# Optimization experiments

Measured on AMD Instinct MI355X. Metric: run time of the kernel, lower is better.

## Reference

```python
import jax, jax.numpy as jnp
import numpy as np

N_NODES = 50000
N_EDGES = 800000
HIDDEN = 128
IN_DIM = 128
OUT_DIM = 1
N_LAYERS = 4
N_GRAPHS = 32
LN_EPS = 1e-5


def setup_inputs() -> dict:
    key = jax.random.key(0)
    ks = jax.random.split(key, 12)
    s = 1.0 / np.sqrt(HIDDEN)
    inp = {
        "x": jax.random.normal(ks[0], (N_NODES, IN_DIM), dtype=jnp.float32),
        "edge_index": jax.random.randint(ks[1], (2, N_EDGES), 0, N_NODES, dtype=jnp.int64),
        "batch": jnp.sort(jax.random.randint(ks[2], (N_NODES,), 0, N_GRAPHS, dtype=jnp.int64)),
        "W_emb": jax.random.normal(ks[3], (HIDDEN, IN_DIM), dtype=jnp.float32) * s,
        "b_emb": jax.random.normal(ks[4], (HIDDEN,), dtype=jnp.float32) * s,
        "W_layers": jax.random.normal(ks[5], (N_LAYERS, HIDDEN, HIDDEN), dtype=jnp.float32) * s,
        "b_layers": jax.random.normal(ks[6], (N_LAYERS, HIDDEN), dtype=jnp.float32) * s,
        "ln_gamma": 1.0 + 0.02 * jax.random.normal(ks[7], (N_LAYERS, HIDDEN), dtype=jnp.float32),
        "ln_beta": 0.02 * jax.random.normal(ks[8], (N_LAYERS, HIDDEN), dtype=jnp.float32),
        "W_out": jax.random.normal(ks[9], (OUT_DIM, HIDDEN), dtype=jnp.float32) * s,
    }
    return inp


def _layer_norm(x, gamma, beta):
    mu = jnp.mean(x, axis=-1, keepdims=True)
    var = jnp.mean(jnp.square(x - mu), axis=-1, keepdims=True)
    return (x - mu) * jax.lax.rsqrt(var + LN_EPS) * gamma + beta


def reference(x, edge_index, batch, W_emb, b_emb, W_layers, b_layers, ln_gamma, ln_beta, W_out):
    n = x.shape[0]
    # add self-loops (PyG GCNConv default)
    loop = jnp.arange(n, dtype=edge_index.dtype)
    row = jnp.concatenate([edge_index[0], loop])  # source nodes
    col = jnp.concatenate([edge_index[1], loop])  # target nodes
    # symmetric normalization: deg over targets
    deg = jax.ops.segment_sum(jnp.ones_like(col, dtype=x.dtype), col, num_segments=n)
    dis = jnp.where(deg > 0, jax.lax.rsqrt(jnp.maximum(deg, 1.0)), 0.0)
    norm = dis[row] * dis[col]  # [E+N]

    h = x @ W_emb.T + b_emb  # embedding layer
    for i in range(N_LAYERS):
        t = h @ W_layers[i].T                      # [N, H] linear first
        msg = t[row] * norm[:, None]               # gather + scale  [E+N, H]
        agg = jax.ops.segment_sum(msg, col, num_segments=n) + b_layers[i]
        h = _layer_norm(h + jax.nn.relu(agg), ln_gamma[i], ln_beta[i])

    out = h @ W_out.T                              # [N, OUT_DIM]
    sums = jax.ops.segment_sum(out, batch, num_segments=N_GRAPHS)
    cnts = jax.ops.segment_sum(jnp.ones((n,), out.dtype), batch, num_segments=N_GRAPHS)
    return sums / jnp.maximum(cnts, 1.0)[:, None]  # [N_GRAPHS, OUT_DIM]
```

## Files before the change

kernel.cpp:

```cpp
#include <hip/hip_runtime.h>
#include <hip/hip_fp16.h>

#define NN 50000
#define NE 800000
#define NH 128
#define NG 32
#define NL 4
#define NB 196
#define WSLOT (NH * NH)

typedef __attribute__((ext_vector_type(8))) short bf16x8;
typedef __attribute__((ext_vector_type(4))) float f32x4;
typedef __attribute__((ext_vector_type(2))) float f32x2;

__device__ inline short f2bf(float x) {
  union { float f; unsigned u; } v;
  v.f = x;
  unsigned r = v.u + 0x7FFF + ((v.u >> 16) & 1);
  return (short)(r >> 16);
}
__device__ inline float bf2f(short s) {
  union { unsigned u; float f; } v;
  v.u = ((unsigned)(unsigned short)s) << 16;
  return v.f;
}

__device__ inline int block_exscan(int v) {
  __shared__ int wsum[4];
  int tid = threadIdx.x, wave = tid >> 6, lane = tid & 63;
  int x = v;
#pragma unroll
  for (int off = 1; off < 64; off <<= 1) {
    int y = __shfl_up(x, off, 64);
    if (lane >= off) x += y;
  }
  if (lane == 63) wsum[wave] = x;
  __syncthreads();
  int wp = 0;
  if (wave > 0) wp += wsum[0];
  if (wave > 1) wp += wsum[1];
  if (wave > 2) wp += wsum[2];
  return wp + x - v;
}

__global__ __launch_bounds__(256) void prep_swizzle(const float* __restrict__ W_emb,
                                                    const float* __restrict__ W_layers,
                                                    short* __restrict__ hi,
                                                    short* __restrict__ lo) {
  int i = blockIdx.x * 256 + threadIdx.x;
  if (i >= 5 * WSLOT) return;
  int slot = i >> 14, f = i & (WSLOT - 1);
  int j = f & 7, lane = (f >> 3) & 63, tt = (f >> 9) & 7, ks = f >> 12;
  int n = tt * 16 + (lane & 15);
  int k = ks * 32 + ((lane >> 4) & 3) * 8 + j;
  const float* W = slot ? (W_layers + (size_t)(slot - 1) * WSLOT) : W_emb;
  float x = W[n * NH + k];
  short hh = f2bf(x);
  hi[i] = hh;
  lo[i] = f2bf(x - bf2f(hh));
}

__global__ __launch_bounds__(256) void hist_kernel(const int* __restrict__ col,
                                                   int* __restrict__ cnt,
                                                   int* __restrict__ rank) {
  int e = blockIdx.x * 256 + threadIdx.x;
  if (e < NE) rank[e] = atomicAdd(&cnt[col[e]], 1);
}

__global__ __launch_bounds__(256) void scan1_kernel(const int* __restrict__ cnt,
                                                    int* __restrict__ bsum,
                                                    float* __restrict__ dis) {
  int i = blockIdx.x * 256 + threadIdx.x;
  int v = (i < NN) ? cnt[i] : 0;
  if (i < NN) dis[i] = rsqrtf((float)(v + 1));
  int lane = threadIdx.x & 63;
  int s = v;
#pragma unroll
  for (int off = 32; off; off >>= 1) s += __shfl_down(s, off, 64);
  __shared__ int ws[4];
  if (lane == 0) ws[threadIdx.x >> 6] = s;
  __syncthreads();
  if (threadIdx.x == 0) bsum[blockIdx.x] = ws[0] + ws[1] + ws[2] + ws[3];
}

__global__ __launch_bounds__(256) void scan2_kernel(const int* __restrict__ bsum,
                                                    int* __restrict__ ebsum) {
  int tid = threadIdx.x;
  int v = (tid < NB) ? bsum[tid] : 0;
  int ex = block_exscan(v);
  if (tid < NB) ebsum[tid] = ex;
}

__global__ __launch_bounds__(256) void scan3_kernel(const int* __restrict__ cnt,
                                                    const int* __restrict__ ebsum,
                                                    int* __restrict__ offs) {
  int i = blockIdx.x * 256 + threadIdx.x;
  int v = (i < NN) ? cnt[i] : 0;
  int ex = block_exscan(v);
  if (i < NN) offs[i] = ebsum[blockIdx.x] + ex;
}

__global__ __launch_bounds__(256) void fill_kernel(const int* __restrict__ row,
                                                   const int* __restrict__ col,
                                                   const int* __restrict__ rank,
                                                   const float* __restrict__ dis,
                                                   const int* __restrict__ offs,
                                                   int2* __restrict__ csr) {
  int e = blockIdx.x * 256 + threadIdx.x;
  if (e < NE) {
    int d = col[e];
    int s = row[e];
    int pos = offs[d] + rank[e];
    csr[pos] = make_int2(s, __float_as_int(dis[s] * dis[d]));
  }
}

template <bool EMB, bool LAST>
__global__ __launch_bounds__(512) void gemm_mfma(const float* __restrict__ Xf,
                                                 const __half* __restrict__ Xh,
                                                 const short* __restrict__ Whi,
                                                 const short* __restrict__ Wlo,
                                                 const float* __restrict__ bias,
                                                 const __half* __restrict__ hprev,
                                                 const float* __restrict__ gamma,
                                                 const float* __restrict__ beta,
                                                 const float* __restrict__ Wout,
                                                 __half* __restrict__ hnew,
                                                 unsigned char* __restrict__ h8,
                                                 float* __restrict__ nodeval) {
  __shared__ short Wh[WSLOT];
  __shared__ short Wl[WSLOT];
  int tid = threadIdx.x;
#pragma unroll
  for (int i = tid * 8; i < WSLOT; i += 512 * 8) {
    *(bf16x8*)&Wh[i] = *(const bf16x8*)(Whi + i);
    *(bf16x8*)&Wl[i] = *(const bf16x8*)(Wlo + i);
  }
  __syncthreads();

  int wave = tid >> 6, lane = tid & 63;
  int quad = lane >> 4, r16 = lane & 15;
  int m0 = blockIdx.x * 128 + wave * 16;
  if (m0 >= NN) return;
  int mA = m0 + r16;

  f32x4 acc[8];
#pragma unroll
  for (int t = 0; t < 8; ++t) acc[t] = (f32x4){0.f, 0.f, 0.f, 0.f};

#pragma unroll
  for (int ks = 0; ks < 4; ++ks) {
    int klane = ks * 32 + quad * 8;
    float af[8];
    if (EMB) {
      const float* xr = Xf + (size_t)mA * NH + klane;
      float4 a0 = *(const float4*)xr;
      float4 a1 = *(const float4*)(xr + 4);
      af[0] = a0.x; af[1] = a0.y; af[2] = a0.z; af[3] = a0.w;
      af[4] = a1.x; af[5] = a1.y; af[6] = a1.z; af[7] = a1.w;
    } else {
      const __half2* xr = (const __half2*)(Xh + (size_t)mA * NH + klane);
#pragma unroll
      for (int q = 0; q < 4; ++q) {
        float2 f = __half22float2(xr[q]);
        af[2 * q] = f.x;
        af[2 * q + 1] = f.y;
      }
    }
    bf16x8 xhi, xlo;
#pragma unroll
    for (int j = 0; j < 8; ++j) {
      short h = f2bf(af[j]);
      xhi[j] = h;
      xlo[j] = f2bf(af[j] - bf2f(h));
    }
#pragma unroll
    for (int t = 0; t < 8; ++t) {
      int fidx = ((ks * 8 + t) * 64 + lane) << 3;
      bf16x8 whi = *(const bf16x8*)&Wh[fidx];
      bf16x8 wlo = *(const bf16x8*)&Wl[fidx];
      acc[t] = __builtin_amdgcn_mfma_f32_16x16x32_bf16(whi, xhi, acc[t], 0, 0, 0);
      acc[t] = __builtin_amdgcn_mfma_f32_16x16x32_bf16(whi, xlo, acc[t], 0, 0, 0);
      acc[t] = __builtin_amdgcn_mfma_f32_16x16x32_bf16(wlo, xhi, acc[t], 0, 0, 0);
    }
  }

  int m = m0 + r16;
  int cb = quad * 4;
  if (EMB) {
#pragma unroll
    for (int t = 0; t < 8; ++t) {
      int ch = t * 16 + cb;
      float4 bb = *(const float4*)(bias + ch);
      float o0 = acc[t][0] + bb.x, o1 = acc[t][1] + bb.y;
      float o2 = acc[t][2] + bb.z, o3 = acc[t][3] + bb.w;
      __half2 p01 = __float22half2_rn(make_float2(o0, o1));
      __half2 p23 = __float22half2_rn(make_float2(o2, o3));
      *(uint2*)(hnew + (size_t)m * NH + ch) =
          make_uint2(*(unsigned*)&p01, *(unsigned*)&p23);
      int v = 0;
      v = __builtin_amdgcn_cvt_pk_fp8_f32(o0, o1, v, 0);
      v = __builtin_amdgcn_cvt_pk_fp8_f32(o2, o3, v, 1);
      ((unsigned*)(h8 + (size_t)m * NH))[t * 4 + quad] = (unsigned)v;
    }
  } else {
    float v[8][4];
    float s = 0.f, s2 = 0.f;
#pragma unroll
    for (int t = 0; t < 8; ++t) {
      int ch = t * 16 + cb;
      float4 bb = *(const float4*)(bias + ch);
      uint2 hp = *(const uint2*)(hprev + (size_t)m * NH + ch);
      float2 h01 = __half22float2(*(__half2*)&hp.x);
      float2 h23 = __half22float2(*(__half2*)&hp.y);
      float hv[4] = {h01.x, h01.y, h23.x, h23.y};
      float bb4[4] = {bb.x, bb.y, bb.z, bb.w};
#pragma unroll
      for (int r = 0; r < 4; ++r) {
        float z = fmaxf(acc[t][r] + bb4[r], 0.f);
        float val = hv[r] + z;
        v[t][r] = val;
        s += val;
        s2 += val * val;
      }
    }
    s += __shfl_xor(s, 16, 64);
    s += __shfl_xor(s, 32, 64);
    s2 += __shfl_xor(s2, 16, 64);
    s2 += __shfl_xor(s2, 32, 64);
    float mean = s * (1.f / 128.f);
    float var = fmaxf(s2 * (1.f / 128.f) - mean * mean, 0.f);
    float inv = rsqrtf(var + 1e-5f);
    float d = 0.f;
#pragma unroll
    for (int t = 0; t < 8; ++t) {
      int ch = t * 16 + cb;
      float4 gv = *(const float4*)(gamma + ch);
      float4 bt = *(const float4*)(beta + ch);
      float o0 = (v[t][0] - mean) * inv * gv.x + bt.x;
      float o1 = (v[t][1] - mean) * inv * gv.y + bt.y;
      float o2 = (v[t][2] - mean) * inv * gv.z + bt.z;
      float o3 = (v[t][3] - mean) * inv * gv.w + bt.w;
      __half2 p01 = __float22half2_rn(make_float2(o0, o1));
      __half2 p23 = __float22half2_rn(make_float2(o2, o3));
      *(uint2*)(hnew + (size_t)m * NH + ch) =
          make_uint2(*(unsigned*)&p01, *(unsigned*)&p23);
      if (!LAST) {
        int pv = 0;
        pv = __builtin_amdgcn_cvt_pk_fp8_f32(o0, o1, pv, 0);
        pv = __builtin_amdgcn_cvt_pk_fp8_f32(o2, o3, pv, 1);
        ((unsigned*)(h8 + (size_t)m * NH))[t * 4 + quad] = (unsigned)pv;
      } else {
        float4 wv = *(const float4*)(Wout + ch);
        d += o0 * wv.x + o1 * wv.y + o2 * wv.z + o3 * wv.w;
      }
    }
    if (LAST) {
      d += __shfl_xor(d, 16, 64);
      d += __shfl_xor(d, 32, 64);
      if (lane < 16) nodeval[m] = d;
    }
  }
}

__global__ __launch_bounds__(256) void aggregate_kernel(
    const unsigned char* __restrict__ h8, __half* __restrict__ agg,
    const float* __restrict__ dis, const int* __restrict__ offs,
    const int* __restrict__ cnt, const int2* __restrict__ csr) {
  int node = blockIdx.x * 4 + (threadIdx.x >> 6);
  int lane = threadIdx.x & 63;
  if (node >= NN) return;
  int hf = lane >> 5;
  int c32 = lane & 31;
  const unsigned* t32 = (const unsigned*)h8;
  float dii = dis[node];
  float sl = dii * dii;
  float4 a = make_float4(0.f, 0.f, 0.f, 0.f);
  if (hf == 0) {
    unsigned raw = t32[(size_t)node * 32 + c32];
    f32x2 lo2 = __builtin_amdgcn_cvt_pk_f32_fp8(raw, 0);
    f32x2 hi2 = __builtin_amdgcn_cvt_pk_f32_fp8(raw, 1);
    a.x = lo2.x * sl; a.y = lo2.y * sl; a.z = hi2.x * sl; a.w = hi2.y * sl;
  }
  int s0 = offs[node];
  int e = cnt[node];
  int j = 0;
  for (; j + 16 <= e; j += 16) {
    int2 p[8];
    unsigned raw[8];
#pragma unroll
    for (int u = 0; u < 8; ++u) p[u] = csr[s0 + j + 2 * u + hf];
#pragma unroll
    for (int u = 0; u < 8; ++u) raw[u] = t32[(size_t)p[u].x * 32 + c32];
#pragma unroll
    for (int u = 0; u < 8; ++u) {
      float w = __int_as_float(p[u].y);
      f32x2 lo2 = __builtin_amdgcn_cvt_pk_f32_fp8(raw[u], 0);
      f32x2 hi2 = __builtin_amdgcn_cvt_pk_f32_fp8(raw[u], 1);
      a.x += lo2.x * w; a.y += lo2.y * w; a.z += hi2.x * w; a.w += hi2.y * w;
    }
  }
  for (; j + 8 <= e; j += 8) {
    int2 p[4];
    unsigned raw[4];
#pragma unroll
    for (int u = 0; u < 4; ++u) p[u] = csr[s0 + j + 2 * u + hf];
#pragma unroll
    for (int u = 0; u < 4; ++u) raw[u] = t32[(size_t)p[u].x * 32 + c32];
#pragma unroll
    for (int u = 0; u < 4; ++u) {
      float w = __int_as_float(p[u].y);
      f32x2 lo2 = __builtin_amdgcn_cvt_pk_f32_fp8(raw[u], 0);
      f32x2 hi2 = __builtin_amdgcn_cvt_pk_f32_fp8(raw[u], 1);
      a.x += lo2.x * w; a.y += lo2.y * w; a.z += hi2.x * w; a.w += hi2.y * w;
    }
  }
  for (; j < e; j += 2) {
    int idx = j + hf;
    int2 p = (idx < e) ? csr[s0 + idx] : make_int2(node, 0);
    float w = __int_as_float(p.y);
    unsigned raw = t32[(size_t)p.x * 32 + c32];
    f32x2 lo2 = __builtin_amdgcn_cvt_pk_f32_fp8(raw, 0);
    f32x2 hi2 = __builtin_amdgcn_cvt_pk_f32_fp8(raw, 1);
    a.x += lo2.x * w; a.y += lo2.y * w; a.z += hi2.x * w; a.w += hi2.y * w;
  }
  a.x += __shfl_down(a.x, 32, 64);
  a.y += __shfl_down(a.y, 32, 64);
  a.z += __shfl_down(a.z, 32, 64);
  a.w += __shfl_down(a.w, 32, 64);
  if (lane < 32) {
    __half2 p01 = __float22half2_rn(make_float2(a.x, a.y));
    __half2 p23 = __float22half2_rn(make_float2(a.z, a.w));
    *(uint2*)(agg + (size_t)node * NH + (c32 << 2)) =
        make_uint2(*(unsigned*)&p01, *(unsigned*)&p23);
  }
}

__global__ __launch_bounds__(256) void reduce_pool_kernel(
    const float* __restrict__ nodeval, const int* __restrict__ batch,
    float* __restrict__ gsum, int* __restrict__ gcnt) {
  __shared__ float bins[NG];
  __shared__ int cbins[NG];
  int tid = threadIdx.x;
  if (tid < NG) {
    bins[tid] = 0.f;
    cbins[tid] = 0;
  }
  __syncthreads();
  int i = blockIdx.x * 256 + tid;
  if (i < NN) {
    int g = batch[i];
    atomicAdd(&bins[g], nodeval[i]);
    atomicAdd(&cbins[g], 1);
  }
  __syncthreads();
  if (tid < NG) {
    if (cbins[tid]) {
      atomicAdd(&gsum[tid], bins[tid]);
      atomicAdd(&gcnt[tid], cbins[tid]);
    }
  }
}

__global__ void finalize_kernel(const float* __restrict__ gsum,
                                const int* __restrict__ gcnt,
                                float* __restrict__ out) {
  int g = threadIdx.x;
  if (g < NG) out[g] = gsum[g] / fmaxf((float)gcnt[g], 1.0f);
}

extern "C" void kernel_launch(void* const* d_in, const int* in_sizes, int n_in,
                              void* d_out, int out_size, void* d_ws, size_t ws_size,
                              hipStream_t stream) {
  const float* x = (const float*)d_in[0];
  const int* eidx = (const int*)d_in[1];
  const int* batch = (const int*)d_in[2];
  const float* W_emb = (const float*)d_in[3];
  const float* b_emb = (const float*)d_in[4];
  const float* W_layers = (const float*)d_in[5];
  const float* b_layers = (const float*)d_in[6];
  const float* ln_gamma = (const float*)d_in[7];
  const float* ln_beta = (const float*)d_in[8];
  const float* W_out = (const float*)d_in[9];
  float* out = (float*)d_out;

  char* ws = (char*)d_ws;
  unsigned char* h8 = (unsigned char*)ws; ws += (size_t)NN * NH;
  __half* h = (__half*)ws;      ws += (size_t)NN * NH * 2;
  __half* agg = (__half*)ws;    ws += (size_t)NN * NH * 2;
  short* Whi = (short*)ws;      ws += (size_t)5 * WSLOT * 2;
  short* Wlo = (short*)ws;      ws += (size_t)5 * WSLOT * 2;
  float* dis = (float*)ws;      ws += (size_t)NN * 4;
  int2* csr = (int2*)ws;        ws += (size_t)NE * 8;
  int* rank = (int*)ws;         ws += (size_t)NE * 4;
  int* offs = (int*)ws;         ws += (size_t)NN * 4;
  float* nodeval = (float*)ws;  ws += (size_t)NN * 4;
  int* bsum = (int*)ws;         ws += (size_t)NB * 4;
  int* ebsum = (int*)ws;        ws += (size_t)NB * 4;
  char* zero_base = ws;
  int* cnt = (int*)ws;          ws += (size_t)NN * 4;
  float* gsum = (float*)ws;     ws += (size_t)NG * 4;
  int* gcnt = (int*)ws;         ws += (size_t)NG * 4;
  size_t zero_bytes = (size_t)(ws - zero_base);
  hipMemsetAsync(zero_base, 0, zero_bytes, stream);

  const int* erow = eidx;
  const int* ecol = eidx + NE;

  prep_swizzle<<<(5 * WSLOT + 255) / 256, 256, 0, stream>>>(W_emb, W_layers, Whi,
                                                            Wlo);
  hist_kernel<<<(NE + 255) / 256, 256, 0, stream>>>(ecol, cnt, rank);
  scan1_kernel<<<NB, 256, 0, stream>>>(cnt, bsum, dis);
  scan2_kernel<<<1, 256, 0, stream>>>(bsum, ebsum);
  scan3_kernel<<<NB, 256, 0, stream>>>(cnt, ebsum, offs);
  fill_kernel<<<(NE + 255) / 256, 256, 0, stream>>>(erow, ecol, rank, dis, offs,
                                                    csr);
  int gblk = (NN + 127) / 128;
  gemm_mfma<true, false><<<gblk, 512, 0, stream>>>(
      x, nullptr, Whi, Wlo, b_emb, nullptr, nullptr, nullptr, nullptr, h, h8,
      nullptr);
  for (int l = 0; l < NL; ++l) {
    aggregate_kernel<<<(NN + 3) / 4, 256, 0, stream>>>(h8, agg, dis, offs, cnt,
                                                       csr);
    const short* wh = Whi + (size_t)(l + 1) * WSLOT;
    const short* wl = Wlo + (size_t)(l + 1) * WSLOT;
    const float* bl = b_layers + (size_t)l * NH;
    const float* gl = ln_gamma + (size_t)l * NH;
    const float* be = ln_beta + (size_t)l * NH;
    if (l == NL - 1)
      gemm_mfma<false, true><<<gblk, 512, 0, stream>>>(
          nullptr, agg, wh, wl, bl, h, gl, be, W_out, h, h8, nodeval);
    else
      gemm_mfma<false, false><<<gblk, 512, 0, stream>>>(
          nullptr, agg, wh, wl, bl, h, gl, be, nullptr, h, h8, nullptr);
  }
  reduce_pool_kernel<<<(NN + 255) / 256, 256, 0, stream>>>(nodeval, batch, gsum,
                                                           gcnt);
  finalize_kernel<<<1, 64, 0, stream>>>(gsum, gcnt, out);
}
```

Measured before the change: 377.6 us.

## Fuse neighbor aggregation into the layer GEMM and merge setup kernels

Removes the separate aggregate kernel. Each layer kernel now gathers the fp8 neighbor rows for its own 16 nodes per wave directly into MFMA operand registers, using a permuted fp8 layout (pdw), then runs the GEMM plus LayerNorm epilogue. This drops the fp16 agg buffer round trip and several launches. The h8 buffer is double-buffered to avoid read/write races across blocks. Setup kernels are merged (prep with hist, scan2 with scan3, finalize into reduce via a last-block flag). The risk is that the per-lane gather, one node per lane with 32 bytes each, is less coalesced and more register-heavy than the old wave-per-node aggregation.

```diff
diff --git a/kernel.cpp b/kernel.cpp
--- a/kernel.cpp
+++ b/kernel.cpp
@@ -7,6 +7,8 @@
 #define NG 32
 #define NL 4
 #define NB 196
+#define PREPB 320
+#define HISTB 3125
 #define WSLOT (NH * NH)
 
 typedef __attribute__((ext_vector_type(8))) short bf16x8;
@@ -25,6 +27,26 @@
   return v.f;
 }
 
+__device__ inline int pdw(int t, int quad) {
+  return (((2 * t + (quad >> 1)) & 3) << 3) + ((t >> 1) << 1) + (quad & 1);
+}
+
+__device__ inline void fp8row_fma(float (&ag)[4][8], uint4 qa, uint4 qb,
+                                  float w) {
+  const unsigned dw[8] = {qa.x, qa.y, qa.z, qa.w, qb.x, qb.y, qb.z, qb.w};
+#pragma unroll
+  for (int ks = 0; ks < 4; ++ks) {
+    f32x2 u0 = __builtin_amdgcn_cvt_pk_f32_fp8(dw[2 * ks], 0);
+    f32x2 u1 = __builtin_amdgcn_cvt_pk_f32_fp8(dw[2 * ks], 1);
+    f32x2 u2 = __builtin_amdgcn_cvt_pk_f32_fp8(dw[2 * ks + 1], 0);
+    f32x2 u3 = __builtin_amdgcn_cvt_pk_f32_fp8(dw[2 * ks + 1], 1);
+    ag[ks][0] += u0.x * w; ag[ks][1] += u0.y * w;
+    ag[ks][2] += u1.x * w; ag[ks][3] += u1.y * w;
+    ag[ks][4] += u2.x * w; ag[ks][5] += u2.y * w;
+    ag[ks][6] += u3.x * w; ag[ks][7] += u3.y * w;
+  }
+}
+
 __device__ inline int block_exscan(int v) {
   __shared__ int wsum[4];
   int tid = threadIdx.x, wave = tid >> 6, lane = tid & 63;
@@ -43,28 +65,26 @@
   return wp + x - v;
 }
 
-__global__ __launch_bounds__(256) void prep_swizzle(const float* __restrict__ W_emb,
-                                                    const float* __restrict__ W_layers,
-                                                    short* __restrict__ hi,
-                                                    short* __restrict__ lo) {
-  int i = blockIdx.x * 256 + threadIdx.x;
-  if (i >= 5 * WSLOT) return;
-  int slot = i >> 14, f = i & (WSLOT - 1);
-  int j = f & 7, lane = (f >> 3) & 63, tt = (f >> 9) & 7, ks = f >> 12;
-  int n = tt * 16 + (lane & 15);
-  int k = ks * 32 + ((lane >> 4) & 3) * 8 + j;
-  const float* W = slot ? (W_layers + (size_t)(slot - 1) * WSLOT) : W_emb;
-  float x = W[n * NH + k];
-  short hh = f2bf(x);
-  hi[i] = hh;
-  lo[i] = f2bf(x - bf2f(hh));
-}
-
-__global__ __launch_bounds__(256) void hist_kernel(const int* __restrict__ col,
-                                                   int* __restrict__ cnt,
-                                                   int* __restrict__ rank) {
-  int e = blockIdx.x * 256 + threadIdx.x;
-  if (e < NE) rank[e] = atomicAdd(&cnt[col[e]], 1);
+__global__ __launch_bounds__(256) void prep_hist_kernel(
+    const float* __restrict__ W_emb, const float* __restrict__ W_layers,
+    short* __restrict__ hi, short* __restrict__ lo, const int* __restrict__ col,
+    int* __restrict__ cnt, int* __restrict__ rank) {
+  if (blockIdx.x < PREPB) {
+    int i = blockIdx.x * 256 + threadIdx.x;
+    if (i >= 5 * WSLOT) return;
+    int slot = i >> 14, f = i & (WSLOT - 1);
+    int j = f & 7, lane = (f >> 3) & 63, tt = (f >> 9) & 7, ks = f >> 12;
+    int n = tt * 16 + (lane & 15);
+    int k = ks * 32 + ((lane >> 4) & 3) * 8 + j;
+    const float* W = slot ? (W_layers + (size_t)(slot - 1) * WSLOT) : W_emb;
+    float x = W[n * NH + k];
+    short hh = f2bf(x);
+    hi[i] = hh;
+    lo[i] = f2bf(x - bf2f(hh));
+  } else {
+    int e = (blockIdx.x - PREPB) * 256 + threadIdx.x;
+    if (e < NE) rank[e] = atomicAdd(&cnt[col[e]], 1);
+  }
 }
 
 __global__ __launch_bounds__(256) void scan1_kernel(const int* __restrict__ cnt,
@@ -83,21 +103,24 @@
   if (threadIdx.x == 0) bsum[blockIdx.x] = ws[0] + ws[1] + ws[2] + ws[3];
 }
 
-__global__ __launch_bounds__(256) void scan2_kernel(const int* __restrict__ bsum,
-                                                    int* __restrict__ ebsum) {
+__global__ __launch_bounds__(256) void scan3b_kernel(const int* __restrict__ cnt,
+                                                     const int* __restrict__ bsum,
+                                                     int* __restrict__ offs) {
+  __shared__ int ws2[4];
   int tid = threadIdx.x;
-  int v = (tid < NB) ? bsum[tid] : 0;
-  int ex = block_exscan(v);
-  if (tid < NB) ebsum[tid] = ex;
-}
-
-__global__ __launch_bounds__(256) void scan3_kernel(const int* __restrict__ cnt,
-                                                    const int* __restrict__ ebsum,
-                                                    int* __restrict__ offs) {
-  int i = blockIdx.x * 256 + threadIdx.x;
-  int v = (i < NN) ? cnt[i] : 0;
-  int ex = block_exscan(v);
-  if (i < NN) offs[i] = ebsum[blockIdx.x] + ex;
+  int b = blockIdx.x;
+  int v = (tid < NB && tid < b) ? bsum[tid] : 0;
+  int lane = tid & 63;
+  int s = v;
+#pragma unroll
+  for (int off = 32; off; off >>= 1) s += __shfl_down(s, off, 64);
+  if (lane == 0) ws2[tid >> 6] = s;
+  __syncthreads();
+  int bo = ws2[0] + ws2[1] + ws2[2] + ws2[3];
+  int i = b * 256 + tid;
+  int c = (i < NN) ? cnt[i] : 0;
+  int ex = block_exscan(c);
+  if (i < NN) offs[i] = bo + ex;
 }
 
 __global__ __launch_bounds__(256) void fill_kernel(const int* __restrict__ row,
@@ -115,19 +138,12 @@
   }
 }
 
-template <bool EMB, bool LAST>
-__global__ __launch_bounds__(512) void gemm_mfma(const float* __restrict__ Xf,
-                                                 const __half* __restrict__ Xh,
-                                                 const short* __restrict__ Whi,
-                                                 const short* __restrict__ Wlo,
-                                                 const float* __restrict__ bias,
-                                                 const __half* __restrict__ hprev,
-                                                 const float* __restrict__ gamma,
-                                                 const float* __restrict__ beta,
-                                                 const float* __restrict__ Wout,
-                                                 __half* __restrict__ hnew,
-                                                 unsigned char* __restrict__ h8,
-                                                 float* __restrict__ nodeval) {
+__global__ __launch_bounds__(512) void emb_gemm(const float* __restrict__ Xf,
+                                                const short* __restrict__ Whi,
+                                                const short* __restrict__ Wlo,
+                                                const float* __restrict__ bias,
+                                                __half* __restrict__ hnew,
+                                                unsigned char* __restrict__ h8) {
   __shared__ short Wh[WSLOT];
   __shared__ short Wl[WSLOT];
   int tid = threadIdx.x;
@@ -151,22 +167,10 @@
 #pragma unroll
   for (int ks = 0; ks < 4; ++ks) {
     int klane = ks * 32 + quad * 8;
-    float af[8];
-    if (EMB) {
-      const float* xr = Xf + (size_t)mA * NH + klane;
-      float4 a0 = *(const float4*)xr;
-      float4 a1 = *(const float4*)(xr + 4);
-      af[0] = a0.x; af[1] = a0.y; af[2] = a0.z; af[3] = a0.w;
-      af[4] = a1.x; af[5] = a1.y; af[6] = a1.z; af[7] = a1.w;
-    } else {
-      const __half2* xr = (const __half2*)(Xh + (size_t)mA * NH + klane);
-#pragma unroll
-      for (int q = 0; q < 4; ++q) {
-        float2 f = __half22float2(xr[q]);
-        af[2 * q] = f.x;
-        af[2 * q + 1] = f.y;
-      }
-    }
+    const float* xr = Xf + (size_t)mA * NH + klane;
+    float4 a0 = *(const float4*)xr;
+    float4 a1 = *(const float4*)(xr + 4);
+    float af[8] = {a0.x, a0.y, a0.z, a0.w, a1.x, a1.y, a1.z, a1.w};
     bf16x8 xhi, xlo;
 #pragma unroll
     for (int j = 0; j < 8; ++j) {
@@ -187,160 +191,175 @@
 
   int m = m0 + r16;
   int cb = quad * 4;
-  if (EMB) {
+#pragma unroll
+  for (int t = 0; t < 8; ++t) {
+    int ch = t * 16 + cb;
+    float4 bb = *(const float4*)(bias + ch);
+    float o0 = acc[t][0] + bb.x, o1 = acc[t][1] + bb.y;
+    float o2 = acc[t][2] + bb.z, o3 = acc[t][3] + bb.w;
+    __half2 p01 = __float22half2_rn(make_float2(o0, o1));
+    __half2 p23 = __float22half2_rn(make_float2(o2, o3));
+    *(uint2*)(hnew + (size_t)m * NH + ch) =
+        make_uint2(*(unsigned*)&p01, *(unsigned*)&p23);
+    int v = 0;
+    v = __builtin_amdgcn_cvt_pk_fp8_f32(o0, o1, v, 0);
+    v = __builtin_amdgcn_cvt_pk_fp8_f32(o2, o3, v, 1);
+    ((unsigned*)(h8 + (size_t)m * NH))[pdw(t, quad)] = (unsigned)v;
+  }
+}
+
+template <bool LAST>
+__global__ __launch_bounds__(512) void layer_fused(
+    const unsigned char* __restrict__ h8in, const short* __restrict__ Whi,
+    const short* __restrict__ Wlo, const float* __restrict__ bias,
+    const __half* __restrict__ hprev, const float* __restrict__ gamma,
+    const float* __restrict__ beta, const float* __restrict__ Wout,
+    const float* __restrict__ dis, const int* __restrict__ offs,
+    const int* __restrict__ cnt, const int2* __restrict__ csr,
+    __half* __restrict__ hnew, unsigned char* __restrict__ h8out,
+    float* __restrict__ nodeval) {
+  __shared__ short Wh[WSLOT];
+  __shared__ short Wl[WSLOT];
+  int tid = threadIdx.x;
+#pragma unroll
+  for (int i = tid * 8; i < WSLOT; i += 512 * 8) {
+    *(bf16x8*)&Wh[i] = *(const bf16x8*)(Whi + i);
+    *(bf16x8*)&Wl[i] = *(const bf16x8*)(Wlo + i);
+  }
+
+  int wave = tid >> 6, lane = tid & 63;
+  int quad = lane >> 4, r16 = lane & 15;
+  int m0 = blockIdx.x * 128 + wave * 16;
+  bool active = m0 < NN;
+  int nd = active ? m0 + r16 : 0;
+
+  float ag[4][8];
+#pragma unroll
+  for (int ks = 0; ks < 4; ++ks)
+#pragma unroll
+    for (int j = 0; j < 8; ++j) ag[ks][j] = 0.f;
+
+  const char* rb = (const char*)h8in + quad * 32;
+  {
+    float dii = dis[nd];
+    const uint4* rp = (const uint4*)(rb + (size_t)nd * NH);
+    uint4 qa = rp[0], qb = rp[1];
+    fp8row_fma(ag, qa, qb, dii * dii);
+  }
+  int s0 = offs[nd];
+  int e = active ? cnt[nd] : 0;
+  int j = 0;
+  for (; j + 2 <= e; j += 2) {
+    int2 p0 = csr[s0 + j], p1 = csr[s0 + j + 1];
+    const uint4* r0 = (const uint4*)(rb + (size_t)p0.x * NH);
+    const uint4* r1 = (const uint4*)(rb + (size_t)p1.x * NH);
+    uint4 a0 = r0[0], b0 = r0[1];
+    uint4 a1 = r1[0], b1 = r1[1];
+    fp8row_fma(ag, a0, b0, __int_as_float(p0.y));
+    fp8row_fma(ag, a1, b1, __int_as_float(p1.y));
+  }
+  if (j < e) {
+    int2 p0 = csr[s0 + j];
+    const uint4* r0 = (const uint4*)(rb + (size_t)p0.x * NH);
+    uint4 a0 = r0[0], b0 = r0[1];
+    fp8row_fma(ag, a0, b0, __int_as_float(p0.y));
+  }
+
+  __syncthreads();
+
+  if (!active) return;
+
+  f32x4 acc[8];
+#pragma unroll
+  for (int t = 0; t < 8; ++t) acc[t] = (f32x4){0.f, 0.f, 0.f, 0.f};
+
+#pragma unroll
+  for (int ks = 0; ks < 4; ++ks) {
+    bf16x8 xhi, xlo;
+#pragma unroll
+    for (int q = 0; q < 8; ++q) {
+      short hh = f2bf(ag[ks][q]);
+      xhi[q] = hh;
+      xlo[q] = f2bf(ag[ks][q] - bf2f(hh));
+    }
 #pragma unroll
     for (int t = 0; t < 8; ++t) {
-      int ch = t * 16 + cb;
-      float4 bb = *(const float4*)(bias + ch);
-      float o0 = acc[t][0] + bb.x, o1 = acc[t][1] + bb.y;
-      float o2 = acc[t][2] + bb.z, o3 = acc[t][3] + bb.w;
+      int fidx = ((ks * 8 + t) * 64 + lane) << 3;
+      bf16x8 whi = *(const bf16x8*)&Wh[fidx];
+      bf16x8 wlo = *(const bf16x8*)&Wl[fidx];
+      acc[t] = __builtin_amdgcn_mfma_f32_16x16x32_bf16(whi, xhi, acc[t], 0, 0, 0);
+      acc[t] = __builtin_amdgcn_mfma_f32_16x16x32_bf16(whi, xlo, acc[t], 0, 0, 0);
+      acc[t] = __builtin_amdgcn_mfma_f32_16x16x32_bf16(wlo, xhi, acc[t], 0, 0, 0);
+    }
+  }
+
+  int m = m0 + r16;
+  int cb = quad * 4;
+  float vv[8][4];
+  float s = 0.f, s2 = 0.f;
+#pragma unroll
+  for (int t = 0; t < 8; ++t) {
+    int ch = t * 16 + cb;
+    float4 bb = *(const float4*)(bias + ch);
+    uint2 hp = *(const uint2*)(hprev + (size_t)m * NH + ch);
+    float2 h01 = __half22float2(*(__half2*)&hp.x);
+    float2 h23 = __half22float2(*(__half2*)&hp.y);
+    float hv[4] = {h01.x, h01.y, h23.x, h23.y};
+    float bb4[4] = {bb.x, bb.y, bb.z, bb.w};
+#pragma unroll
+    for (int r = 0; r < 4; ++r) {
+      float z = fmaxf(acc[t][r] + bb4[r], 0.f);
+      float val = hv[r] + z;
+      vv[t][r] = val;
+      s += val;
+      s2 += val * val;
+    }
+  }
+  s += __shfl_xor(s, 16, 64);
+  s += __shfl_xor(s, 32, 64);
+  s2 += __shfl_xor(s2, 16, 64);
+  s2 += __shfl_xor(s2, 32, 64);
+  float mean = s * (1.f / 128.f);
+  float var = fmaxf(s2 * (1.f / 128.f) - mean * mean, 0.f);
+  float inv = rsqrtf(var + 1e-5f);
+  float d = 0.f;
+#pragma unroll
+  for (int t = 0; t < 8; ++t) {
+    int ch = t * 16 + cb;
+    float4 gv = *(const float4*)(gamma + ch);
+    float4 bt = *(const float4*)(beta + ch);
+    float o0 = (vv[t][0] - mean) * inv * gv.x + bt.x;
+    float o1 = (vv[t][1] - mean) * inv * gv.y + bt.y;
+    float o2 = (vv[t][2] - mean) * inv * gv.z + bt.z;
+    float o3 = (vv[t][3] - mean) * inv * gv.w + bt.w;
+    if (!LAST) {
       __half2 p01 = __float22half2_rn(make_float2(o0, o1));
       __half2 p23 = __float22half2_rn(make_float2(o2, o3));
       *(uint2*)(hnew + (size_t)m * NH + ch) =
           make_uint2(*(unsigned*)&p01, *(unsigned*)&p23);
-      int v = 0;
-      v = __builtin_amdgcn_cvt_pk_fp8_f32(o0, o1, v, 0);
-      v = __builtin_amdgcn_cvt_pk_fp8_f32(o2, o3, v, 1);
-      ((unsigned*)(h8 + (size_t)m * NH))[t * 4 + quad] = (unsigned)v;
-    }
-  } else {
-    float v[8][4];
-    float s = 0.f, s2 = 0.f;
-#pragma unroll
-    for (int t = 0; t < 8; ++t) {
-      int ch = t * 16 + cb;
-      float4 bb = *(const float4*)(bias + ch);
-      uint2 hp = *(const uint2*)(hprev + (size_t)m * NH + ch);
-      float2 h01 = __half22float2(*(__half2*)&hp.x);
-      float2 h23 = __half22float2(*(__half2*)&hp.y);
-      float hv[4] = {h01.x, h01.y, h23.x, h23.y};
-      float bb4[4] = {bb.x, bb.y, bb.z, bb.w};
-#pragma unroll
-      for (int r = 0; r < 4; ++r) {
-        float z = fmaxf(acc[t][r] + bb4[r], 0.f);
-        float val = hv[r] + z;
-        v[t][r] = val;
-        s += val;
-        s2 += val * val;
-      }
-    }
-    s += __shfl_xor(s, 16, 64);
-    s += __shfl_xor(s, 32, 64);
-    s2 += __shfl_xor(s2, 16, 64);
-    s2 += __shfl_xor(s2, 32, 64);
-    float mean = s * (1.f / 128.f);
-    float var = fmaxf(s2 * (1.f / 128.f) - mean * mean, 0.f);
-    float inv = rsqrtf(var + 1e-5f);
-    float d = 0.f;
-#pragma unroll
-    for (int t = 0; t < 8; ++t) {
-      int ch = t * 16 + cb;
-      float4 gv = *(const float4*)(gamma + ch);
-      float4 bt = *(const float4*)(beta + ch);
-      float o0 = (v[t][0] - mean) * inv * gv.x + bt.x;
-      float o1 = (v[t][1] - mean) * inv * gv.y + bt.y;
-      float o2 = (v[t][2] - mean) * inv * gv.z + bt.z;
-      float o3 = (v[t][3] - mean) * inv * gv.w + bt.w;
-      __half2 p01 = __float22half2_rn(make_float2(o0, o1));
-      __half2 p23 = __float22half2_rn(make_float2(o2, o3));
-      *(uint2*)(hnew + (size_t)m * NH + ch) =
-          make_uint2(*(unsigned*)&p01, *(unsigned*)&p23);
-      if (!LAST) {
-        int pv = 0;
-        pv = __builtin_amdgcn_cvt_pk_fp8_f32(o0, o1, pv, 0);
-        pv = __builtin_amdgcn_cvt_pk_fp8_f32(o2, o3, pv, 1);
-        ((unsigned*)(h8 + (size_t)m * NH))[t * 4 + quad] = (unsigned)pv;
-      } else {
-        float4 wv = *(const float4*)(Wout + ch);
-        d += o0 * wv.x + o1 * wv.y + o2 * wv.z + o3 * wv.w;
-      }
-    }
-    if (LAST) {
-      d += __shfl_xor(d, 16, 64);
-      d += __shfl_xor(d, 32, 64);
-      if (lane < 16) nodeval[m] = d;
-    }
-  }
-}
-
-__global__ __launch_bounds__(256) void aggregate_kernel(
-    const unsigned char* __restrict__ h8, __half* __restrict__ agg,
-    const float* __restrict__ dis, const int* __restrict__ offs,
-    const int* __restrict__ cnt, const int2* __restrict__ csr) {
-  int node = blockIdx.x * 4 + (threadIdx.x >> 6);
-  int lane = threadIdx.x & 63;
-  if (node >= NN) return;
-  int hf = lane >> 5;
-  int c32 = lane & 31;
-  const unsigned* t32 = (const unsigned*)h8;
-  float dii = dis[node];
-  float sl = dii * dii;
-  float4 a = make_float4(0.f, 0.f, 0.f, 0.f);
-  if (hf == 0) {
-    unsigned raw = t32[(size_t)node * 32 + c32];
-    f32x2 lo2 = __builtin_amdgcn_cvt_pk_f32_fp8(raw, 0);
-    f32x2 hi2 = __builtin_amdgcn_cvt_pk_f32_fp8(raw, 1);
-    a.x = lo2.x * sl; a.y = lo2.y * sl; a.z = hi2.x * sl; a.w = hi2.y * sl;
-  }
-  int s0 = offs[node];
-  int e = cnt[node];
-  int j = 0;
-  for (; j + 16 <= e; j += 16) {
-    int2 p[8];
-    unsigned raw[8];
-#pragma unroll
-    for (int u = 0; u < 8; ++u) p[u] = csr[s0 + j + 2 * u + hf];
-#pragma unroll
-    for (int u = 0; u < 8; ++u) raw[u] = t32[(size_t)p[u].x * 32 + c32];
-#pragma unroll
-    for (int u = 0; u < 8; ++u) {
-      float w = __int_as_float(p[u].y);
-      f32x2 lo2 = __builtin_amdgcn_cvt_pk_f32_fp8(raw[u], 0);
-      f32x2 hi2 = __builtin_amdgcn_cvt_pk_f32_fp8(raw[u], 1);
-      a.x += lo2.x * w; a.y += lo2.y * w; a.z += hi2.x * w; a.w += hi2.y * w;
-    }
-  }
-  for (; j + 8 <= e; j += 8) {
-    int2 p[4];
-    unsigned raw[4];
-#pragma unroll
-    for (int u = 0; u < 4; ++u) p[u] = csr[s0 + j + 2 * u + hf];
-#pragma unroll
-    for (int u = 0; u < 4; ++u) raw[u] = t32[(size_t)p[u].x * 32 + c32];
-#pragma unroll
-    for (int u = 0; u < 4; ++u) {
-      float w = __int_as_float(p[u].y);
-      f32x2 lo2 = __builtin_amdgcn_cvt_pk_f32_fp8(raw[u], 0);
-      f32x2 hi2 = __builtin_amdgcn_cvt_pk_f32_fp8(raw[u], 1);
-      a.x += lo2.x * w; a.y += lo2.y * w; a.z += hi2.x * w; a.w += hi2.y * w;
-    }
-  }
-  for (; j < e; j += 2) {
-    int idx = j + hf;
-    int2 p = (idx < e) ? csr[s0 + idx] : make_int2(node, 0);
-    float w = __int_as_float(p.y);
-    unsigned raw = t32[(size_t)p.x * 32 + c32];
-    f32x2 lo2 = __builtin_amdgcn_cvt_pk_f32_fp8(raw, 0);
-    f32x2 hi2 = __builtin_amdgcn_cvt_pk_f32_fp8(raw, 1);
-    a.x += lo2.x * w; a.y += lo2.y * w; a.z += hi2.x * w; a.w += hi2.y * w;
-  }
-  a.x += __shfl_down(a.x, 32, 64);
-  a.y += __shfl_down(a.y, 32, 64);
-  a.z += __shfl_down(a.z, 32, 64);
-  a.w += __shfl_down(a.w, 32, 64);
-  if (lane < 32) {
-    __half2 p01 = __float22half2_rn(make_float2(a.x, a.y));
-    __half2 p23 = __float22half2_rn(make_float2(a.z, a.w));
-    *(uint2*)(agg + (size_t)node * NH + (c32 << 2)) =
-        make_uint2(*(unsigned*)&p01, *(unsigned*)&p23);
+      int pv = 0;
+      pv = __builtin_amdgcn_cvt_pk_fp8_f32(o0, o1, pv, 0);
+      pv = __builtin_amdgcn_cvt_pk_fp8_f32(o2, o3, pv, 1);
+      ((unsigned*)(h8out + (size_t)m * NH))[pdw(t, quad)] = (unsigned)pv;
+    } else {
+      float4 wv = *(const float4*)(Wout + ch);
+      d += o0 * wv.x + o1 * wv.y + o2 * wv.z + o3 * wv.w;
+    }
+  }
+  if (LAST) {
+    d += __shfl_xor(d, 16, 64);
+    d += __shfl_xor(d, 32, 64);
+    if (lane < 16) nodeval[m] = d;
   }
 }
 
 __global__ __launch_bounds__(256) void reduce_pool_kernel(
     const float* __restrict__ nodeval, const int* __restrict__ batch,
-    float* __restrict__ gsum, int* __restrict__ gcnt) {
+    float* __restrict__ gsum, int* __restrict__ gcnt, int* __restrict__ done,
+    float* __restrict__ out) {
   __shared__ float bins[NG];
   __shared__ int cbins[NG];
+  __shared__ int lastflag;
   int tid = threadIdx.x;
   if (tid < NG) {
     bins[tid] = 0.f;
@@ -354,19 +373,18 @@
     atomicAdd(&cbins[g], 1);
   }
   __syncthreads();
-  if (tid < NG) {
-    if (cbins[tid]) {
-      atomicAdd(&gsum[tid], bins[tid]);
-      atomicAdd(&gcnt[tid], cbins[tid]);
-    }
-  }
-}
-
-__global__ void finalize_kernel(const float* __restrict__ gsum,
-                                const int* __restrict__ gcnt,
-                                float* __restrict__ out) {
-  int g = threadIdx.x;
-  if (g < NG) out[g] = gsum[g] / fmaxf((float)gcnt[g], 1.0f);
+  if (tid < NG && cbins[tid]) {
+    atomicAdd(&gsum[tid], bins[tid]);
+    atomicAdd(&gcnt[tid], cbins[tid]);
+  }
+  __threadfence();
+  if (tid == 0) lastflag = (atomicAdd(done, 1) == (int)gridDim.x - 1);
+  __syncthreads();
+  if (lastflag && tid < NG) {
+    float sv = atomicAdd(&gsum[tid], 0.f);
+    int cv = atomicAdd(&gcnt[tid], 0);
+    out[tid] = sv / fmaxf((float)cv, 1.0f);
+  }
 }
 
 extern "C" void kernel_launch(void* const* d_in, const int* in_sizes, int n_in,
@@ -385,9 +403,9 @@
   float* out = (float*)d_out;
 
   char* ws = (char*)d_ws;
-  unsigned char* h8 = (unsigned char*)ws; ws += (size_t)NN * NH;
+  unsigned char* h8a = (unsigned char*)ws; ws += (size_t)NN * NH;
+  unsigned char* h8b = (unsigned char*)ws; ws += (size_t)NN * NH;
   __half* h = (__half*)ws;      ws += (size_t)NN * NH * 2;
-  __half* agg = (__half*)ws;    ws += (size_t)NN * NH * 2;
   short* Whi = (short*)ws;      ws += (size_t)5 * WSLOT * 2;
   short* Wlo = (short*)ws;      ws += (size_t)5 * WSLOT * 2;
   float* dis = (float*)ws;      ws += (size_t)NN * 4;
@@ -396,45 +414,42 @@
   int* offs = (int*)ws;         ws += (size_t)NN * 4;
   float* nodeval = (float*)ws;  ws += (size_t)NN * 4;
   int* bsum = (int*)ws;         ws += (size_t)NB * 4;
-  int* ebsum = (int*)ws;        ws += (size_t)NB * 4;
   char* zero_base = ws;
   int* cnt = (int*)ws;          ws += (size_t)NN * 4;
   float* gsum = (float*)ws;     ws += (size_t)NG * 4;
   int* gcnt = (int*)ws;         ws += (size_t)NG * 4;
+  int* done = (int*)ws;         ws += 64;
   size_t zero_bytes = (size_t)(ws - zero_base);
   hipMemsetAsync(zero_base, 0, zero_bytes, stream);
 
   const int* erow = eidx;
   const int* ecol = eidx + NE;
 
-  prep_swizzle<<<(5 * WSLOT + 255) / 256, 256, 0, stream>>>(W_emb, W_layers, Whi,
-                                                            Wlo);
-  hist_kernel<<<(NE + 255) / 256, 256, 0, stream>>>(ecol, cnt, rank);
+  prep_hist_kernel<<<PREPB + HISTB, 256, 0, stream>>>(W_emb, W_layers, Whi, Wlo,
+                                                      ecol, cnt, rank);
   scan1_kernel<<<NB, 256, 0, stream>>>(cnt, bsum, dis);
-  scan2_kernel<<<1, 256, 0, stream>>>(bsum, ebsum);
-  scan3_kernel<<<NB, 256, 0, stream>>>(cnt, ebsum, offs);
-  fill_kernel<<<(NE + 255) / 256, 256, 0, stream>>>(erow, ecol, rank, dis, offs,
-                                                    csr);
+  scan3b_kernel<<<NB, 256, 0, stream>>>(cnt, bsum, offs);
+  fill_kernel<<<HISTB, 256, 0, stream>>>(erow, ecol, rank, dis, offs, csr);
+
   int gblk = (NN + 127) / 128;
-  gemm_mfma<true, false><<<gblk, 512, 0, stream>>>(
-      x, nullptr, Whi, Wlo, b_emb, nullptr, nullptr, nullptr, nullptr, h, h8,
-      nullptr);
+  emb_gemm<<<gblk, 512, 0, stream>>>(x, Whi, Wlo, b_emb, h, h8a);
   for (int l = 0; l < NL; ++l) {
-    aggregate_kernel<<<(NN + 3) / 4, 256, 0, stream>>>(h8, agg, dis, offs, cnt,
-                                                       csr);
     const short* wh = Whi + (size_t)(l + 1) * WSLOT;
     const short* wl = Wlo + (size_t)(l + 1) * WSLOT;
     const float* bl = b_layers + (size_t)l * NH;
     const float* gl = ln_gamma + (size_t)l * NH;
     const float* be = ln_beta + (size_t)l * NH;
+    const unsigned char* hin = (l & 1) ? h8b : h8a;
+    unsigned char* hout = (l & 1) ? h8a : h8b;
     if (l == NL - 1)
-      gemm_mfma<false, true><<<gblk, 512, 0, stream>>>(
-          nullptr, agg, wh, wl, bl, h, gl, be, W_out, h, h8, nodeval);
+      layer_fused<true><<<gblk, 512, 0, stream>>>(
+          hin, wh, wl, bl, h, gl, be, W_out, dis, offs, cnt, csr, h, nullptr,
+          nodeval);
     else
-      gemm_mfma<false, false><<<gblk, 512, 0, stream>>>(
-          nullptr, agg, wh, wl, bl, h, gl, be, nullptr, h, h8, nullptr);
-  }
-  reduce_pool_kernel<<<(NN + 255) / 256, 256, 0, stream>>>(nodeval, batch, gsum,
-                                                           gcnt);
-  finalize_kernel<<<1, 64, 0, stream>>>(gsum, gcnt, out);
-}
+      layer_fused<false><<<gblk, 512, 0, stream>>>(
+          hin, wh, wl, bl, h, gl, be, nullptr, dis, offs, cnt, csr, h, hout,
+          nullptr);
+  }
+  reduce_pool_kernel<<<NB, 256, 0, stream>>>(nodeval, batch, gsum, gcnt, done,
+                                             out);
+}
```

Result: faster. 330.0 us (-12.6%).
